# Performance work log

Hardware: AMD Instinct MI355X
Metric: run time of the kernel (lower is better)

The kernel has to match this reference:

```python
import jax, jax.numpy as jnp
import numpy as np

B, N, K = 16, 4096, 32

def setup_inputs() -> dict:
    key = jax.random.key(0)
    k0, k1, k2, k3, k4, k5 = jax.random.split(key, 6)
    frames_rot = jax.random.normal(k0, (B, N, 3, 3), jnp.float32)
    frames_trans = jax.random.normal(k1, (B, N, 3), jnp.float32)
    pair_rot = jax.random.normal(k2, (B, N, K, 3, 3), jnp.float32)
    pair_trans = jax.random.normal(k3, (B, N, K, 3), jnp.float32)
    confidences = jax.random.uniform(k4, (B, N, K, 1), jnp.float32)
    topology = jax.random.randint(k5, (B, N, K), 0, N, jnp.int32)
    return {"frames_rot": frames_rot, "frames_trans": frames_trans,
            "pair_rot": pair_rot, "pair_trans": pair_trans,
            "confidences": confidences, "topology": topology}


def _proj_with_svd(m):
    """Kabsch projection of batched [..., 3, 3] matrices onto SO(3) (det=+1)."""
    u, s, vh = jnp.linalg.svd(m, full_matrices=False)
    V = jnp.swapaxes(vh, -1, -2)
    d = jnp.sign(jnp.linalg.det(jnp.matmul(V, jnp.swapaxes(u, -1, -2))))  # [...]
    d3 = jnp.concatenate([jnp.ones(d.shape + (2,), m.dtype), d[..., None]], axis=-1)  # diag(1,1,d)
    # rot = V @ diag(1,1,d) @ u^T
    return jnp.einsum('...ik,...k,...jk->...ij', V, d3, u)


def reference(frames_rot, frames_trans, pair_rot, pair_trans, confidences, topology):
    # gather neighbor frames T_j: [B,N,K,3,3] / [B,N,K,3]
    gather = jax.vmap(lambda f, t: f[t])
    Tj_rot = gather(frames_rot, topology)
    Tj_trans = gather(frames_trans, topology)

    # normalized confidences p_ij over neighbors K
    w = jnp.squeeze(confidences, axis=-1)             # [B,N,K]
    p = w / jnp.sum(w, axis=2, keepdims=True)         # [B,N,K]

    # compose rigids: T_j * T_ji
    comp_rot = jnp.einsum('bnkij,bnkjl->bnkil', Tj_rot, pair_rot)                 # [B,N,K,3,3]
    comp_trans = jnp.einsum('bnkij,bnkj->bnki', Tj_rot, pair_trans) + Tj_trans    # [B,N,K,3]

    # confidence-weighted average over neighbors
    avg_rot = jnp.einsum('bnk,bnkij->bnij', p, comp_rot)    # [B,N,3,3]
    avg_trans = jnp.einsum('bnk,bnki->bni', p, comp_trans)  # [B,N,3]

    # project averaged rot onto SO(3), then invert (transpose) as in the module
    rot = _proj_with_svd(avg_rot)
    rot_inv = jnp.swapaxes(rot, -1, -2)                     # invert_rots of a rotation

    # pack (rot 9 + trans 3) -> [B,N,12]
    return jnp.concatenate([rot_inv.reshape(B, N, 9), avg_trans], axis=-1)
```

## Files before the change

### kernel.cpp

```cpp
#include <hip/hip_runtime.h>
#include <math.h>

#define N_RES 4096
#define KNB 32
#define BN_TOTAL 65536

typedef float v4f __attribute__((ext_vector_type(4)));
typedef int v4i __attribute__((ext_vector_type(4)));

template <int p, int q>
__device__ __forceinline__ void jacobi_rot(float S[3][3], float V[3][3]) {
    float apq = S[p][q];
    if (fabsf(apq) > 1e-20f) {
        float app = S[p][p], aqq = S[q][q];
        float tau = (aqq - app) / (2.0f * apq);
        float tt = (tau >= 0.0f ? 1.0f : -1.0f) / (fabsf(tau) + sqrtf(1.0f + tau * tau));
        float c = 1.0f / sqrtf(1.0f + tt * tt);
        float s = tt * c;
#pragma unroll
        for (int i = 0; i < 3; i++) {
            float Sip = S[i][p], Siq = S[i][q];
            S[i][p] = c * Sip - s * Siq;
            S[i][q] = s * Sip + c * Siq;
        }
#pragma unroll
        for (int i = 0; i < 3; i++) {
            float Spi = S[p][i], Sqi = S[q][i];
            S[p][i] = c * Spi - s * Sqi;
            S[q][i] = s * Spi + c * Sqi;
        }
#pragma unroll
        for (int i = 0; i < 3; i++) {
            float Vip = V[i][p], Viq = V[i][q];
            V[i][p] = c * Vip - s * Viq;
            V[i][q] = s * Vip + c * Viq;
        }
    }
}

template <int A, int Bc>
__device__ __forceinline__ void sort_pair(float lam[3], float V[3][3]) {
    if (lam[A] < lam[Bc]) {
        float tl = lam[A]; lam[A] = lam[Bc]; lam[Bc] = tl;
#pragma unroll
        for (int i = 0; i < 3; i++) {
            float tv = V[i][A]; V[i][A] = V[i][Bc]; V[i][Bc] = tv;
        }
    }
}

__device__ __forceinline__ void project_and_store(const float M[3][3],
                                                  float t0, float t1, float t2,
                                                  float* outp) {
    float S[3][3];
#pragma unroll
    for (int i = 0; i < 3; i++)
#pragma unroll
        for (int j = 0; j < 3; j++)
            S[i][j] = M[0][i] * M[0][j] + M[1][i] * M[1][j] + M[2][i] * M[2][j];
    float V[3][3] = {{1, 0, 0}, {0, 1, 0}, {0, 0, 1}};

#pragma unroll
    for (int sweep = 0; sweep < 4; sweep++) {
        jacobi_rot<0, 1>(S, V);
        jacobi_rot<0, 2>(S, V);
        jacobi_rot<1, 2>(S, V);
    }

    float lam[3] = {S[0][0], S[1][1], S[2][2]};
    sort_pair<0, 1>(lam, V);
    sort_pair<1, 2>(lam, V);
    sort_pair<0, 1>(lam, V);

    float detV = V[0][0] * (V[1][1] * V[2][2] - V[1][2] * V[2][1]) -
                 V[0][1] * (V[1][0] * V[2][2] - V[1][2] * V[2][0]) +
                 V[0][2] * (V[1][0] * V[2][1] - V[1][1] * V[2][0]);
    if (detV < 0.0f) { V[0][2] = -V[0][2]; V[1][2] = -V[1][2]; V[2][2] = -V[2][2]; }

    float Bm[3][3];
#pragma unroll
    for (int i = 0; i < 3; i++)
#pragma unroll
        for (int j = 0; j < 3; j++)
            Bm[i][j] = M[i][0] * V[0][j] + M[i][1] * V[1][j] + M[i][2] * V[2][j];

    float u0[3] = {Bm[0][0], Bm[1][0], Bm[2][0]};
    float n0 = u0[0] * u0[0] + u0[1] * u0[1] + u0[2] * u0[2];
    float rn0 = 1.0f / sqrtf(fmaxf(n0, 1e-24f));
    u0[0] *= rn0; u0[1] *= rn0; u0[2] *= rn0;

    float b1[3] = {Bm[0][1], Bm[1][1], Bm[2][1]};
    float d01 = u0[0] * b1[0] + u0[1] * b1[1] + u0[2] * b1[2];
    float u1[3] = {b1[0] - d01 * u0[0], b1[1] - d01 * u0[1], b1[2] - d01 * u0[2]};
    float n1 = u1[0] * u1[0] + u1[1] * u1[1] + u1[2] * u1[2];
    float rn1 = 1.0f / sqrtf(fmaxf(n1, 1e-24f));
    u1[0] *= rn1; u1[1] *= rn1; u1[2] *= rn1;

    float u2[3] = {u0[1] * u1[2] - u0[2] * u1[1],
                   u0[2] * u1[0] - u0[0] * u1[2],
                   u0[0] * u1[1] - u0[1] * u1[0]};

    float R[9];
#pragma unroll
    for (int i = 0; i < 3; i++) {
        float Ui0 = (i == 0 ? u0[0] : (i == 1 ? u0[1] : u0[2]));
        float Ui1 = (i == 0 ? u1[0] : (i == 1 ? u1[1] : u1[2]));
        float Ui2 = (i == 0 ? u2[0] : (i == 1 ? u2[1] : u2[2]));
#pragma unroll
        for (int j = 0; j < 3; j++)
            R[i * 3 + j] = Ui0 * V[j][0] + Ui1 * V[j][1] + Ui2 * V[j][2];
    }

    v4f* o4 = (v4f*)outp;
    o4[0] = (v4f){R[0], R[1], R[2], R[3]};
    o4[1] = (v4f){R[4], R[5], R[6], R[7]};
    o4[2] = (v4f){R[8], t0, t1, t2};
}

__global__ __launch_bounds__(256) void repack_kernel(
    const float* __restrict__ frames_rot,
    const float* __restrict__ frames_trans,
    float* __restrict__ pk)
{
    int row = blockIdx.x * 256 + threadIdx.x;
    const float* fr = frames_rot + (size_t)row * 9;
    const float* ft = frames_trans + (size_t)row * 3;
    v4f a = {fr[0], fr[1], fr[2], fr[3]};
    v4f b = {fr[4], fr[5], fr[6], fr[7]};
    v4f c = {fr[8], ft[0], ft[1], ft[2]};
    v4f* o = (v4f*)(pk + (size_t)row * 16);
    o[0] = a; o[1] = b; o[2] = c;
}

#define LDS_E_STRIDE 148

__global__ __launch_bounds__(256) void accum_kernel(
    const float* __restrict__ pk,
    const float* __restrict__ pair_rot,
    const float* __restrict__ pair_trans,
    const float* __restrict__ conf,
    const int* __restrict__ topo,
    float* __restrict__ acc)
{
    __shared__ float lds_rot[32 * LDS_E_STRIDE];

    int tid = threadIdx.x;
    int bid = blockIdx.x;

    int xcd = bid & 7;
    int slot = bid >> 3;
    int batch = xcd + ((slot >> 7) << 3);
    int chunkidx = slot & 127;
    int elem0 = batch * N_RES + chunkidx * 32;

    int e = tid >> 3;
    int t = tid & 7;
    int elem_g = elem0 + e;

    float wl[4];
    int jl[4];
    float ptl[12];
#pragma unroll
    for (int s = 0; s < 4; s++) {
        size_t nidx = (size_t)elem_g * KNB + t + 8 * s;
        wl[s] = __builtin_nontemporal_load(conf + nidx);
        jl[s] = __builtin_nontemporal_load(topo + nidx);
#pragma unroll
        for (int c = 0; c < 3; c++)
            ptl[s * 3 + c] = __builtin_nontemporal_load(pair_trans + nidx * 3 + c);
    }

    const float* pkb = pk + (size_t)batch * N_RES * 16;
    v4f g0a, g0b, g0c, g1a, g1b, g1c;
    {
        const v4f* r0 = (const v4f*)(pkb + (size_t)jl[0] * 16);
        const v4f* r1 = (const v4f*)(pkb + (size_t)jl[1] * 16);
        g0a = r0[0]; g0b = r0[1]; g0c = r0[2];
        g1a = r1[0]; g1b = r1[1]; g1c = r1[2];
    }

    float Macc[9] = {0, 0, 0, 0, 0, 0, 0, 0, 0};
    float tacc[3] = {0, 0, 0};
    float wsum = wl[0] + wl[1] + wl[2] + wl[3];

#pragma unroll
    for (int ch = 0; ch < 2; ch++) {
        for (int i = tid; i < 1152; i += 256) {
            int se = i / 36;
            int r = i - se * 36;
            const v4f* gp = (const v4f*)(pair_rot +
                ((size_t)(elem0 + se) * KNB + ch * 16) * 9) + r;
            v4f v = __builtin_nontemporal_load(gp);
            *(v4f*)(lds_rot + se * LDS_E_STRIDE + r * 4) = v;
        }
        __syncthreads();

#pragma unroll
        for (int sc = 0; sc < 2; sc++) {
            int s = 2 * ch + sc;
            float w = wl[s];
            const float* lp = lds_rot + e * LDS_E_STRIDE + 9 * (t + 8 * sc);
            float pr[9];
#pragma unroll
            for (int c = 0; c < 9; c++) pr[c] = lp[c];

            v4f fa = (s & 1) ? g1a : g0a;
            v4f fb = (s & 1) ? g1b : g0b;
            v4f fc = (s & 1) ? g1c : g0c;
            float r[9] = {fa.x, fa.y, fa.z, fa.w, fb.x, fb.y, fb.z, fb.w, fc.x};
            float tj[3] = {fc.y, fc.z, fc.w};
            const float* pt = ptl + s * 3;

#pragma unroll
            for (int i = 0; i < 3; i++) {
#pragma unroll
                for (int l = 0; l < 3; l++) {
                    float cij = r[i * 3 + 0] * pr[0 * 3 + l] +
                                r[i * 3 + 1] * pr[1 * 3 + l] +
                                r[i * 3 + 2] * pr[2 * 3 + l];
                    Macc[i * 3 + l] += w * cij;
                }
                float ct = r[i * 3 + 0] * pt[0] + r[i * 3 + 1] * pt[1] +
                           r[i * 3 + 2] * pt[2] + tj[i];
                tacc[i] += w * ct;
            }

            if (ch == 0) {
                const v4f* rn = (const v4f*)(pkb + (size_t)jl[2 + sc] * 16);
                if (sc == 0) { g0a = rn[0]; g0b = rn[1]; g0c = rn[2]; }
                else         { g1a = rn[0]; g1b = rn[1]; g1c = rn[2]; }
            }
        }
        if (ch == 0) __syncthreads();
    }

#pragma unroll
    for (int st = 1; st <= 4; st <<= 1) {
#pragma unroll
        for (int i = 0; i < 9; i++) Macc[i] += __shfl_xor(Macc[i], st);
#pragma unroll
        for (int i = 0; i < 3; i++) tacc[i] += __shfl_xor(tacc[i], st);
        wsum += __shfl_xor(wsum, st);
    }

    if (t == 0) {
        v4f* o = (v4f*)(acc + (size_t)elem_g * 16);
        o[0] = (v4f){Macc[0], Macc[1], Macc[2], Macc[3]};
        o[1] = (v4f){Macc[4], Macc[5], Macc[6], Macc[7]};
        o[2] = (v4f){Macc[8], tacc[0], tacc[1], tacc[2]};
        o[3] = (v4f){wsum, 0.0f, 0.0f, 0.0f};
    }
}

__global__ __launch_bounds__(256) void solve_kernel(
    const float* __restrict__ acc,
    float* __restrict__ out)
{
    int elem = blockIdx.x * 256 + threadIdx.x;
    const v4f* a4 = (const v4f*)(acc + (size_t)elem * 16);
    v4f A0 = a4[0], A1 = a4[1], A2 = a4[2], A3 = a4[3];
    float inv_w = 1.0f / fmaxf(A3.x, 1e-20f);
    float M[3][3] = {{A0.x * inv_w, A0.y * inv_w, A0.z * inv_w},
                     {A0.w * inv_w, A1.x * inv_w, A1.y * inv_w},
                     {A1.z * inv_w, A1.w * inv_w, A2.x * inv_w}};
    float t0 = A2.y * inv_w, t1 = A2.z * inv_w, t2 = A2.w * inv_w;
    project_and_store(M, t0, t1, t2, out + (size_t)elem * 12);
}

__global__ __launch_bounds__(256) void fused_kernel(
    const float* __restrict__ frames_rot, const float* __restrict__ frames_trans,
    const float* __restrict__ pair_rot, const float* __restrict__ pair_trans,
    const float* __restrict__ conf, const int* __restrict__ topo,
    float* __restrict__ out)
{
    int tid = threadIdx.x;
    int bid = blockIdx.x;
    int xcd = bid & 7;
    int slot = bid >> 3;
    int batch = xcd + ((slot >> 7) << 3);
    int chunk = slot & 127;
    int elem = batch * N_RES + chunk * 32 + (tid >> 3);
    int t = tid & 7;

    const float* fr_b = frames_rot + (size_t)batch * N_RES * 9;
    const float* ft_b = frames_trans + (size_t)batch * N_RES * 3;

    size_t kbase = (size_t)elem * KNB + (size_t)t * 4;
    const v4f* pr4 = (const v4f*)(pair_rot + kbase * 9);
    const v4f* pt4 = (const v4f*)(pair_trans + kbase * 3);
    const v4f* cf4 = (const v4f*)(conf + kbase);
    const v4i* tp4 = (const v4i*)(topo + kbase);

    float prl[36];
#pragma unroll
    for (int i = 0; i < 9; i++) {
        v4f v = __builtin_nontemporal_load(pr4 + i);
        prl[4 * i] = v.x; prl[4 * i + 1] = v.y; prl[4 * i + 2] = v.z; prl[4 * i + 3] = v.w;
    }
    float ptl[12];
#pragma unroll
    for (int i = 0; i < 3; i++) {
        v4f v = __builtin_nontemporal_load(pt4 + i);
        ptl[4 * i] = v.x; ptl[4 * i + 1] = v.y; ptl[4 * i + 2] = v.z; ptl[4 * i + 3] = v.w;
    }
    v4f wv = __builtin_nontemporal_load(cf4);
    float wl[4] = {wv.x, wv.y, wv.z, wv.w};
    v4i jv = __builtin_nontemporal_load(tp4);
    int jl[4] = {jv.x, jv.y, jv.z, jv.w};

    float Macc[9] = {0, 0, 0, 0, 0, 0, 0, 0, 0};
    float tacc[3] = {0, 0, 0};
    float wsum = 0.0f;

#pragma unroll
    for (int kk = 0; kk < 4; kk++) {
        int j = jl[kk];
        const float* Rj = fr_b + j * 9;
        const float* Tj = ft_b + j * 3;
        float r[9];
#pragma unroll
        for (int i = 0; i < 9; i++) r[i] = Rj[i];
        float tj[3];
#pragma unroll
        for (int i = 0; i < 3; i++) tj[i] = Tj[i];
        float w = wl[kk];
        const float* pr = prl + kk * 9;
        const float* pt = ptl + kk * 3;
#pragma unroll
        for (int i = 0; i < 3; i++) {
#pragma unroll
            for (int l = 0; l < 3; l++) {
                float cij = r[i * 3] * pr[l] + r[i * 3 + 1] * pr[3 + l] + r[i * 3 + 2] * pr[6 + l];
                Macc[i * 3 + l] += w * cij;
            }
            float ct = r[i * 3] * pt[0] + r[i * 3 + 1] * pt[1] + r[i * 3 + 2] * pt[2] + tj[i];
            tacc[i] += w * ct;
        }
        wsum += w;
    }

#pragma unroll
    for (int st = 1; st <= 4; st <<= 1) {
#pragma unroll
        for (int i = 0; i < 9; i++) Macc[i] += __shfl_xor(Macc[i], st);
#pragma unroll
        for (int i = 0; i < 3; i++) tacc[i] += __shfl_xor(tacc[i], st);
        wsum += __shfl_xor(wsum, st);
    }

    float inv_w = 1.0f / fmaxf(wsum, 1e-20f);
    float M[3][3];
#pragma unroll
    for (int i = 0; i < 3; i++)
#pragma unroll
        for (int j = 0; j < 3; j++) M[i][j] = Macc[i * 3 + j] * inv_w;

    if (t == 0)
        project_and_store(M, tacc[0] * inv_w, tacc[1] * inv_w, tacc[2] * inv_w,
                          out + (size_t)elem * 12);
}

extern "C" void kernel_launch(void* const* d_in, const int* in_sizes, int n_in,
                              void* d_out, int out_size, void* d_ws, size_t ws_size,
                              hipStream_t stream) {
    const float* frames_rot = (const float*)d_in[0];
    const float* frames_trans = (const float*)d_in[1];
    const float* pair_rot = (const float*)d_in[2];
    const float* pair_trans = (const float*)d_in[3];
    const float* conf = (const float*)d_in[4];
    const int* topo = (const int*)d_in[5];
    float* out = (float*)d_out;

    const size_t PK_BYTES = (size_t)BN_TOTAL * 16 * sizeof(float);
    const size_t need = 2 * PK_BYTES;

    if (ws_size >= need) {
        float* pk = (float*)d_ws;
        float* acc = pk + (size_t)BN_TOTAL * 16;
        hipLaunchKernelGGL(repack_kernel, dim3(BN_TOTAL / 256), dim3(256), 0, stream,
                           frames_rot, frames_trans, pk);
        hipLaunchKernelGGL(accum_kernel, dim3(BN_TOTAL / 32), dim3(256), 0, stream,
                           pk, pair_rot, pair_trans, conf, topo, acc);
        hipLaunchKernelGGL(solve_kernel, dim3(BN_TOTAL / 256), dim3(256), 0, stream,
                           acc, out);
    } else {
        hipLaunchKernelGGL(fused_kernel, dim3(BN_TOTAL * 8 / 256), dim3(256), 0, stream,
                           frames_rot, frames_trans, pair_rot, pair_trans, conf, topo, out);
    }
}
```

Before: 175.6 us.

## Stage pair_trans and gathered neighbor frames through LDS in four chunks

The accumulation kernel now processes neighbors in four chunks of 8 instead of two chunks of 16. Each chunk stages pair_rot, pair_trans (as coalesced vector loads) and the gathered neighbor frames into LDS before computing. The frame gather uses wave shuffles of the topology indices so that four lanes cooperatively fetch each 64-byte packed frame. This is meant to coalesce the scattered gathers and the stride-3 pair_trans loads, at the cost of more barriers and extra LDS traffic. The repack kernel also zero-fills the padding word of each packed row.

```diff
diff --git a/kernel.cpp b/kernel.cpp
--- a/kernel.cpp
+++ b/kernel.cpp
@@ -7,6 +7,13 @@
 
 typedef float v4f __attribute__((ext_vector_type(4)));
 typedef int v4i __attribute__((ext_vector_type(4)));
+
+#define ROT_STRIDE 76
+#define TRN_STRIDE 28
+#define ROT_OFF 0
+#define TRN_OFF (32 * ROT_STRIDE)
+#define FRM_OFF (TRN_OFF + 32 * TRN_STRIDE)
+#define LDS_TOTAL (FRM_OFF + 256 * 16)
 
 template <int p, int q>
 __device__ __forceinline__ void jacobi_rot(float S[3][3], float V[3][3]) {
@@ -125,14 +132,12 @@
     int row = blockIdx.x * 256 + threadIdx.x;
     const float* fr = frames_rot + (size_t)row * 9;
     const float* ft = frames_trans + (size_t)row * 3;
-    v4f a = {fr[0], fr[1], fr[2], fr[3]};
-    v4f b = {fr[4], fr[5], fr[6], fr[7]};
-    v4f c = {fr[8], ft[0], ft[1], ft[2]};
     v4f* o = (v4f*)(pk + (size_t)row * 16);
-    o[0] = a; o[1] = b; o[2] = c;
-}
-
-#define LDS_E_STRIDE 148
+    o[0] = (v4f){fr[0], fr[1], fr[2], fr[3]};
+    o[1] = (v4f){fr[4], fr[5], fr[6], fr[7]};
+    o[2] = (v4f){fr[8], ft[0], ft[1], ft[2]};
+    o[3] = (v4f){0.0f, 0.0f, 0.0f, 0.0f};
+}
 
 __global__ __launch_bounds__(256) void accum_kernel(
     const float* __restrict__ pk,
@@ -142,7 +147,7 @@
     const int* __restrict__ topo,
     float* __restrict__ acc)
 {
-    __shared__ float lds_rot[32 * LDS_E_STRIDE];
+    __shared__ float lds[LDS_TOTAL];
 
     int tid = threadIdx.x;
     int bid = blockIdx.x;
@@ -155,61 +160,66 @@
 
     int e = tid >> 3;
     int t = tid & 7;
+    int lane = tid & 63;
+    int wbase = (tid >> 6) * 64;
     int elem_g = elem0 + e;
 
     float wl[4];
     int jl[4];
-    float ptl[12];
 #pragma unroll
     for (int s = 0; s < 4; s++) {
-        size_t nidx = (size_t)elem_g * KNB + t + 8 * s;
+        size_t nidx = (size_t)elem_g * KNB + s * 8 + t;
         wl[s] = __builtin_nontemporal_load(conf + nidx);
         jl[s] = __builtin_nontemporal_load(topo + nidx);
-#pragma unroll
-        for (int c = 0; c < 3; c++)
-            ptl[s * 3 + c] = __builtin_nontemporal_load(pair_trans + nidx * 3 + c);
     }
 
     const float* pkb = pk + (size_t)batch * N_RES * 16;
-    v4f g0a, g0b, g0c, g1a, g1b, g1c;
-    {
-        const v4f* r0 = (const v4f*)(pkb + (size_t)jl[0] * 16);
-        const v4f* r1 = (const v4f*)(pkb + (size_t)jl[1] * 16);
-        g0a = r0[0]; g0b = r0[1]; g0c = r0[2];
-        g1a = r1[0]; g1b = r1[1]; g1c = r1[2];
-    }
 
     float Macc[9] = {0, 0, 0, 0, 0, 0, 0, 0, 0};
     float tacc[3] = {0, 0, 0};
     float wsum = wl[0] + wl[1] + wl[2] + wl[3];
 
 #pragma unroll
-    for (int ch = 0; ch < 2; ch++) {
-        for (int i = tid; i < 1152; i += 256) {
-            int se = i / 36;
-            int r = i - se * 36;
+    for (int ch = 0; ch < 4; ch++) {
+        for (int i = tid; i < 576; i += 256) {
+            int se = i / 18;
+            int r = i - se * 18;
             const v4f* gp = (const v4f*)(pair_rot +
-                ((size_t)(elem0 + se) * KNB + ch * 16) * 9) + r;
+                ((size_t)(elem0 + se) * KNB + ch * 8) * 9) + r;
             v4f v = __builtin_nontemporal_load(gp);
-            *(v4f*)(lds_rot + se * LDS_E_STRIDE + r * 4) = v;
+            *(v4f*)(lds + ROT_OFF + se * ROT_STRIDE + r * 4) = v;
+        }
+        if (tid < 192) {
+            int se = tid / 6;
+            int r = tid - se * 6;
+            const v4f* gp = (const v4f*)(pair_trans +
+                ((size_t)(elem0 + se) * KNB + ch * 8) * 3) + r;
+            v4f v = __builtin_nontemporal_load(gp);
+            *(v4f*)(lds + TRN_OFF + se * TRN_STRIDE + r * 4) = v;
+        }
+#pragma unroll
+        for (int q = 0; q < 4; q++) {
+            int fw = q * 16 + (lane >> 2);
+            int sl = lane & 3;
+            int j = __shfl(jl[ch], fw);
+            v4f v = *((const v4f*)(pkb + (size_t)j * 16) + sl);
+            *(v4f*)(lds + FRM_OFF + (wbase + fw) * 16 + sl * 4) = v;
         }
         __syncthreads();
 
-#pragma unroll
-        for (int sc = 0; sc < 2; sc++) {
-            int s = 2 * ch + sc;
-            float w = wl[s];
-            const float* lp = lds_rot + e * LDS_E_STRIDE + 9 * (t + 8 * sc);
+        {
+            float w = wl[ch];
+            const float* lp = lds + ROT_OFF + e * ROT_STRIDE + 9 * t;
             float pr[9];
 #pragma unroll
             for (int c = 0; c < 9; c++) pr[c] = lp[c];
-
-            v4f fa = (s & 1) ? g1a : g0a;
-            v4f fb = (s & 1) ? g1b : g0b;
-            v4f fc = (s & 1) ? g1c : g0c;
+            const float* tp = lds + TRN_OFF + e * TRN_STRIDE + 3 * t;
+            float pt0 = tp[0], pt1 = tp[1], pt2 = tp[2];
+
+            const v4f* fp = (const v4f*)(lds + FRM_OFF + (e * 8 + t) * 16);
+            v4f fa = fp[0], fb = fp[1], fc = fp[2];
             float r[9] = {fa.x, fa.y, fa.z, fa.w, fb.x, fb.y, fb.z, fb.w, fc.x};
             float tj[3] = {fc.y, fc.z, fc.w};
-            const float* pt = ptl + s * 3;
 
 #pragma unroll
             for (int i = 0; i < 3; i++) {
@@ -220,18 +230,12 @@
                                 r[i * 3 + 2] * pr[2 * 3 + l];
                     Macc[i * 3 + l] += w * cij;
                 }
-                float ct = r[i * 3 + 0] * pt[0] + r[i * 3 + 1] * pt[1] +
-                           r[i * 3 + 2] * pt[2] + tj[i];
+                float ct = r[i * 3 + 0] * pt0 + r[i * 3 + 1] * pt1 +
+                           r[i * 3 + 2] * pt2 + tj[i];
                 tacc[i] += w * ct;
             }
-
-            if (ch == 0) {
-                const v4f* rn = (const v4f*)(pkb + (size_t)jl[2 + sc] * 16);
-                if (sc == 0) { g0a = rn[0]; g0b = rn[1]; g0c = rn[2]; }
-                else         { g1a = rn[0]; g1b = rn[1]; g1c = rn[2]; }
-            }
-        }
-        if (ch == 0) __syncthreads();
+        }
+        if (ch < 3) __syncthreads();
     }
 
 #pragma unroll
@@ -372,11 +376,12 @@
     float* out = (float*)d_out;
 
     const size_t PK_BYTES = (size_t)BN_TOTAL * 16 * sizeof(float);
-    const size_t need = 2 * PK_BYTES;
+    const size_t ACC_BYTES = (size_t)BN_TOTAL * 16 * sizeof(float);
+    const size_t need = PK_BYTES + ACC_BYTES;
 
     if (ws_size >= need) {
         float* pk = (float*)d_ws;
-        float* acc = pk + (size_t)BN_TOTAL * 16;
+        float* acc = (float*)((char*)d_ws + PK_BYTES);
         hipLaunchKernelGGL(repack_kernel, dim3(BN_TOTAL / 256), dim3(256), 0, stream,
                            frames_rot, frames_trans, pk);
         hipLaunchKernelGGL(accum_kernel, dim3(BN_TOTAL / 32), dim3(256), 0, stream,
```

New measurement: 176.0 us. No clear change (+0.3%).

## Stage pair data in wave-private LDS and drop block barriers

Applied to the files above, without the earlier changes.

The accumulation kernel now gives each wavefront its own LDS slice covering 8 elements. This removes the two block-wide __syncthreads per block. pair_trans is now staged through LDS with coalesced 16-byte loads instead of per-thread strided scalar loads. The change relies on the wave-private LDS write-then-read order being correct without explicit barriers.

```diff
diff --git a/kernel.cpp b/kernel.cpp
--- a/kernel.cpp
+++ b/kernel.cpp
@@ -7,6 +7,11 @@
 
 typedef float v4f __attribute__((ext_vector_type(4)));
 typedef int v4i __attribute__((ext_vector_type(4)));
+
+#define ROT_S 148
+#define TRN_S 52
+#define TRN_BASE (8 * ROT_S)
+#define WLDS (TRN_BASE + 8 * TRN_S)
 
 template <int p, int q>
 __device__ __forceinline__ void jacobi_rot(float S[3][3], float V[3][3]) {
@@ -125,14 +130,11 @@
     int row = blockIdx.x * 256 + threadIdx.x;
     const float* fr = frames_rot + (size_t)row * 9;
     const float* ft = frames_trans + (size_t)row * 3;
-    v4f a = {fr[0], fr[1], fr[2], fr[3]};
-    v4f b = {fr[4], fr[5], fr[6], fr[7]};
-    v4f c = {fr[8], ft[0], ft[1], ft[2]};
     v4f* o = (v4f*)(pk + (size_t)row * 16);
-    o[0] = a; o[1] = b; o[2] = c;
-}
-
-#define LDS_E_STRIDE 148
+    o[0] = (v4f){fr[0], fr[1], fr[2], fr[3]};
+    o[1] = (v4f){fr[4], fr[5], fr[6], fr[7]};
+    o[2] = (v4f){fr[8], ft[0], ft[1], ft[2]};
+}
 
 __global__ __launch_bounds__(256) void accum_kernel(
     const float* __restrict__ pk,
@@ -142,32 +144,32 @@
     const int* __restrict__ topo,
     float* __restrict__ acc)
 {
-    __shared__ float lds_rot[32 * LDS_E_STRIDE];
+    __shared__ float lds[4 * WLDS];
 
     int tid = threadIdx.x;
+    int wid = tid >> 6;
+    int L = tid & 63;
     int bid = blockIdx.x;
 
     int xcd = bid & 7;
     int slot = bid >> 3;
     int batch = xcd + ((slot >> 7) << 3);
-    int chunkidx = slot & 127;
-    int elem0 = batch * N_RES + chunkidx * 32;
-
-    int e = tid >> 3;
-    int t = tid & 7;
+    int within = slot & 127;
+    int elem0 = batch * N_RES + within * 32 + wid * 8;
+
+    int e = L >> 3;
+    int t = L & 7;
     int elem_g = elem0 + e;
+
+    float* wlds = lds + wid * WLDS;
 
     float wl[4];
     int jl[4];
-    float ptl[12];
 #pragma unroll
     for (int s = 0; s < 4; s++) {
-        size_t nidx = (size_t)elem_g * KNB + t + 8 * s;
+        size_t nidx = (size_t)elem_g * KNB + s * 8 + t;
         wl[s] = __builtin_nontemporal_load(conf + nidx);
         jl[s] = __builtin_nontemporal_load(topo + nidx);
-#pragma unroll
-        for (int c = 0; c < 3; c++)
-            ptl[s * 3 + c] = __builtin_nontemporal_load(pair_trans + nidx * 3 + c);
     }
 
     const float* pkb = pk + (size_t)batch * N_RES * 16;
@@ -179,50 +181,56 @@
         g1a = r1[0]; g1b = r1[1]; g1c = r1[2];
     }
 
+    const v4f* rg = (const v4f*)(pair_rot + (size_t)elem0 * (KNB * 9));
+    const v4f* tg = (const v4f*)(pair_trans + (size_t)elem0 * (KNB * 3));
+
     float Macc[9] = {0, 0, 0, 0, 0, 0, 0, 0, 0};
     float tacc[3] = {0, 0, 0};
     float wsum = wl[0] + wl[1] + wl[2] + wl[3];
 
 #pragma unroll
     for (int ch = 0; ch < 2; ch++) {
-        for (int i = tid; i < 1152; i += 256) {
-            int se = i / 36;
-            int r = i - se * 36;
-            const v4f* gp = (const v4f*)(pair_rot +
-                ((size_t)(elem0 + se) * KNB + ch * 16) * 9) + r;
-            v4f v = __builtin_nontemporal_load(gp);
-            *(v4f*)(lds_rot + se * LDS_E_STRIDE + r * 4) = v;
-        }
-        __syncthreads();
+        for (int i = L; i < 288; i += 64) {
+            int e2 = i / 36;
+            int r = i - e2 * 36;
+            v4f v = __builtin_nontemporal_load(rg + e2 * 72 + ch * 36 + r);
+            *(v4f*)(wlds + e2 * ROT_S + 4 * r) = v;
+        }
+        for (int i = L; i < 96; i += 64) {
+            int e2 = i / 12;
+            int r = i - e2 * 12;
+            v4f v = __builtin_nontemporal_load(tg + e2 * 24 + ch * 12 + r);
+            *(v4f*)(wlds + TRN_BASE + e2 * TRN_S + 4 * r) = v;
+        }
 
 #pragma unroll
         for (int sc = 0; sc < 2; sc++) {
             int s = 2 * ch + sc;
             float w = wl[s];
-            const float* lp = lds_rot + e * LDS_E_STRIDE + 9 * (t + 8 * sc);
-            float pr[9];
-#pragma unroll
-            for (int c = 0; c < 9; c++) pr[c] = lp[c];
+            int m = sc * 8 + t;
+            const float* lp = wlds + e * ROT_S + 9 * m;
+            float p[9];
+#pragma unroll
+            for (int c = 0; c < 9; c++) p[c] = lp[c];
+            const float* tp = wlds + TRN_BASE + e * TRN_S + 3 * m;
+            float q0 = tp[0], q1 = tp[1], q2 = tp[2];
 
             v4f fa = (s & 1) ? g1a : g0a;
             v4f fb = (s & 1) ? g1b : g0b;
             v4f fc = (s & 1) ? g1c : g0c;
             float r[9] = {fa.x, fa.y, fa.z, fa.w, fb.x, fb.y, fb.z, fb.w, fc.x};
             float tj[3] = {fc.y, fc.z, fc.w};
-            const float* pt = ptl + s * 3;
 
 #pragma unroll
             for (int i = 0; i < 3; i++) {
 #pragma unroll
                 for (int l = 0; l < 3; l++) {
-                    float cij = r[i * 3 + 0] * pr[0 * 3 + l] +
-                                r[i * 3 + 1] * pr[1 * 3 + l] +
-                                r[i * 3 + 2] * pr[2 * 3 + l];
-                    Macc[i * 3 + l] += w * cij;
+                    Macc[i * 3 + l] += w * (r[i * 3 + 0] * p[0 * 3 + l] +
+                                            r[i * 3 + 1] * p[1 * 3 + l] +
+                                            r[i * 3 + 2] * p[2 * 3 + l]);
                 }
-                float ct = r[i * 3 + 0] * pt[0] + r[i * 3 + 1] * pt[1] +
-                           r[i * 3 + 2] * pt[2] + tj[i];
-                tacc[i] += w * ct;
+                tacc[i] += w * (r[i * 3 + 0] * q0 + r[i * 3 + 1] * q1 +
+                                r[i * 3 + 2] * q2 + tj[i]);
             }
 
             if (ch == 0) {
@@ -231,7 +239,6 @@
                 else         { g1a = rn[0]; g1b = rn[1]; g1c = rn[2]; }
             }
         }
-        if (ch == 0) __syncthreads();
     }
 
 #pragma unroll
@@ -372,11 +379,12 @@
     float* out = (float*)d_out;
 
     const size_t PK_BYTES = (size_t)BN_TOTAL * 16 * sizeof(float);
-    const size_t need = 2 * PK_BYTES;
+    const size_t ACC_BYTES = (size_t)BN_TOTAL * 16 * sizeof(float);
+    const size_t need = PK_BYTES + ACC_BYTES;
 
     if (ws_size >= need) {
         float* pk = (float*)d_ws;
-        float* acc = pk + (size_t)BN_TOTAL * 16;
+        float* acc = (float*)((char*)d_ws + PK_BYTES);
         hipLaunchKernelGGL(repack_kernel, dim3(BN_TOTAL / 256), dim3(256), 0, stream,
                            frames_rot, frames_trans, pk);
         hipLaunchKernelGGL(accum_kernel, dim3(BN_TOTAL / 32), dim3(256), 0, stream,
```

Result: no change. 175.4 us (-0.1%).
